# Kernel tuning notes

Measured on AMD Instinct MI355X. Metric: run time of the kernel, lower is better.

The kernel has to match this reference:

```python
import jax, jax.numpy as jnp
import numpy as np

ALPHA = 0.2      # LeakyReLU negative slope
NEG_INF = -9e15  # mask value from the original code

def setup_inputs() -> dict:
    key = jax.random.key(0)
    k1, k2, k3, k4 = jax.random.split(key, 4)
    B, M, F_IN, F_OUT = 16, 2048, 128, 64
    h = jax.random.normal(k1, (B, M, F_IN), dtype=jnp.float32)
    adj = jax.random.randint(k2, (B, M, M), 0, 2, dtype=jnp.int32)
    W = jax.random.normal(k3, (F_IN, F_OUT), dtype=jnp.float32) * 0.1
    a = jax.random.normal(k4, (2 * F_OUT, 1), dtype=jnp.float32) * 0.1
    return {"h": h, "adj": adj, "W": W, "a": a}

def reference(h, adj, W, a):
    # h: [B,M,Fin], adj: [B,M,M], W: [Fin,E], a: [2E,1]
    Wh = jnp.matmul(h, W)                      # [B,M,E]
    E = Wh.shape[-1]
    a1, a2 = a[:E, 0], a[E:, 0]
    # decompose a^T [Wh_i || Wh_j] = (Wh_i . a1) + (Wh_j . a2)
    f1 = Wh @ a1                               # [B,M] (source/query term)
    f2 = Wh @ a2                               # [B,M] (target/key term)
    e = jax.nn.leaky_relu(f1[:, :, None] + f2[:, None, :], negative_slope=ALPHA)  # [B,M,M]
    scores = jnp.where(adj > 0, e, NEG_INF)
    attn = jax.nn.softmax(scores, axis=-1)     # [B,M,M]  (dropout p=0 / eval mode)
    h_prime = jnp.matmul(attn, Wh)             # [B,M,E]
    return jax.nn.elu(h_prime)                 # concat=True branch
```

## Files before the change

kernel.cpp:

```cpp
#include <hip/hip_runtime.h>


#define M_     2048
#define FIN_   128
#define F_     64
#define ALPHA_ 0.2f
#define HS_    132
#define WT_    132

typedef float  float4_ __attribute__((ext_vector_type(4)));
typedef short  short8  __attribute__((ext_vector_type(8)));
typedef int    int4_   __attribute__((ext_vector_type(4)));
typedef unsigned int u32x4 __attribute__((ext_vector_type(4)));
typedef unsigned short u16;
typedef unsigned int   u32;

static __device__ __forceinline__ u32 cvtpk(float lo, float hi) {
    u32 r;
    asm("v_cvt_pk_bf16_f32 %0, %1, %2" : "=v"(r) : "v"(lo), "v"(hi));
    return r;
}

static __device__ __forceinline__ int4_ ntload4(const int* p) {
    return __builtin_nontemporal_load((const int4_*)p);
}

__global__ __launch_bounds__(256, 4) void k_prep(
    const float* __restrict__ h, const float* __restrict__ W,
    const float* __restrict__ a, u16* __restrict__ hbf,
    float* __restrict__ f1all, float* __restrict__ f2all)
{
    __shared__ float a_s[2 * F_];
    __shared__ float wa1[FIN_], wa2[FIN_];
    __shared__ float hs[32 * HS_];

    const int tid = threadIdx.x;
    const u32 bid = blockIdx.x;
    const u32 lg  = (bid & 7) * 128 + (bid >> 3);
    const int b   = lg >> 6;
    const int t   = lg & 63;

    if (tid < 128) a_s[tid] = a[tid];

    const int tok = tid >> 3, f0 = (tid & 7) * 16;
    const float* hp = h + ((size_t)(b * M_ + t * 32 + tok)) * FIN_ + f0;
    float4_ x0 = *(const float4_*)hp;
    float4_ x1 = *(const float4_*)(hp + 4);
    float4_ x2 = *(const float4_*)(hp + 8);
    float4_ x3 = *(const float4_*)(hp + 12);
    __syncthreads();

    if (tid < FIN_) {
        float s1 = 0.f, s2 = 0.f;
#pragma unroll 8
        for (int n = 0; n < F_; ++n) {
            float wv = W[tid * F_ + n];
            s1 += wv * a_s[n];
            s2 += wv * a_s[F_ + n];
        }
        wa1[tid] = s1;
        wa2[tid] = s2;
    }

    float* hr = hs + tok * HS_ + f0;
    *(float4_*)(hr)      = x0;
    *(float4_*)(hr + 4)  = x1;
    *(float4_*)(hr + 8)  = x2;
    *(float4_*)(hr + 12) = x3;
    __syncthreads();

    {
        const int l = tid & 63, lc = l & 15, q = l >> 4;
        const int nt0 = (tid >> 6) * 2;
        u32x4* ob = (u32x4*)hbf + ((size_t)(b * 64 + t)) * 8 * 64;
#pragma unroll
        for (int ni = 0; ni < 2; ++ni) {
            const int nt = nt0 + ni;
            const float* cp = hs + (q * 8) * HS_ + nt * 16 + lc;
            u32x4 wv;
            wv[0] = cvtpk(cp[0 * HS_], cp[1 * HS_]);
            wv[1] = cvtpk(cp[2 * HS_], cp[3 * HS_]);
            wv[2] = cvtpk(cp[4 * HS_], cp[5 * HS_]);
            wv[3] = cvtpk(cp[6 * HS_], cp[7 * HS_]);
            ob[nt * 64 + l] = wv;
        }
    }

    {
        const int r = tid >> 3, k0 = (tid & 7) * 16;
        const float* rp = hs + r * HS_ + k0;
        float s1 = 0.f, s2 = 0.f;
#pragma unroll
        for (int k = 0; k < 16; ++k) {
            s1 += rp[k] * wa1[k0 + k];
            s2 += rp[k] * wa2[k0 + k];
        }
        s1 += __shfl_xor(s1, 1, 64); s2 += __shfl_xor(s2, 1, 64);
        s1 += __shfl_xor(s1, 2, 64); s2 += __shfl_xor(s2, 2, 64);
        s1 += __shfl_xor(s1, 4, 64); s2 += __shfl_xor(s2, 4, 64);
        if ((tid & 7) == 0) {
            f1all[b * M_ + t * 32 + r] = s1;
            f2all[b * M_ + t * 32 + r] = s2;
        }
    }
}

__global__ __launch_bounds__(256, 2) void k_main(
    const int* __restrict__ adj, const u16* __restrict__ hbf,
    const float* __restrict__ f1all, const float* __restrict__ f2all,
    const float* __restrict__ W, float* __restrict__ out)
{
    __shared__ char  dyn[64 * WT_ * 4];
    __shared__ float dens[64];

    u32x4* lbuf = (u32x4*)dyn;
    float* f2s  = (float*)(dyn + 16384);
    float* Tsum = (float*)dyn;

    const int tid  = threadIdx.x;
    const int w    = tid >> 6;
    const int l    = tid & 63;
    const int lc   = l & 15;
    const int quad = l >> 4;

    const u32 bid = blockIdx.x;
    const u32 lg  = (bid & 7) * 64 + (bid >> 3);
    const int b   = lg >> 5;
    const int i0  = (lg & 31) * 64;

    {
        const int o = tid * 8;
        float4_ v0 = *(const float4_*)(f2all + b * M_ + o);
        float4_ v1 = *(const float4_*)(f2all + b * M_ + o + 4);
        *(float4_*)(f2s + o)     = v0;
        *(float4_*)(f2s + o + 4) = v1;
    }

    const float f1r = f1all[b * M_ + i0 + w * 16 + lc];
    const int* aprow = adj + ((size_t)(b * M_ + i0 + w * 16 + lc)) * M_ + quad * 8;
    const u32x4* hbs = (const u32x4*)hbf + (size_t)b * 32768;

    {
        u32x4 s0 = hbs[tid];
        u32x4 s1 = hbs[256 + tid];
        lbuf[tid]       = s0;
        lbuf[256 + tid] = s1;
    }
    int4_ aA0 = ntload4(aprow);
    int4_ aA1 = ntload4(aprow + 4);
    int4_ aB0 = ntload4(aprow + 32);
    int4_ aB1 = ntload4(aprow + 36);

    __syncthreads();

    float denacc = 0.f;
    float4_ acc[8];
#pragma unroll
    for (int nt = 0; nt < 8; ++nt) acc[nt] = (float4_){0.f, 0.f, 0.f, 0.f};

#define SC(GE, GO, AE, AO, IDX)                                 \
        {                                                       \
            float xe = f1r + (GE); xe = fmaxf(xe, ALPHA_ * xe); \
            float xo = f1r + (GO); xo = fmaxf(xo, ALPHA_ * xo); \
            float ee = ((AE) > 0) ? __expf(xe) : 0.f;           \
            float eo = ((AO) > 0) ? __expf(xo) : 0.f;           \
            u32 pk = cvtpk(ee, eo);                             \
            d += __uint_as_float(pk << 16);                     \
            d += __uint_as_float(pk & 0xFFFF0000u);             \
            pw[IDX] = pk;                                       \
        }

#define STAGE(T, A0, A1)                                                      \
    {                                                                         \
        const int ts = ((T) < 63) ? (T) + 1 : 63;                             \
        const int tp = ((T) < 62) ? (T) + 2 : 63;                             \
        u32x4 s0 = hbs[ts * 512 + tid];                                       \
        u32x4 s1 = hbs[ts * 512 + 256 + tid];                                 \
        __builtin_amdgcn_sched_barrier(0);                                    \
        const u32x4* lc_ = lbuf + ((T) & 1) * 512;                            \
        u32x4 bb[8];                                                          \
        _Pragma("unroll")                                                     \
        for (int nt = 0; nt < 8; ++nt) bb[nt] = lc_[nt * 64 + l];             \
        float4_ g0 = *(const float4_*)(f2s + (T) * 32 + quad * 8);            \
        float4_ g1 = *(const float4_*)(f2s + (T) * 32 + quad * 8 + 4);        \
        u32x4 pw;                                                             \
        float d = 0.f;                                                        \
        SC(g0[0], g0[1], A0[0], A0[1], 0)                                     \
        SC(g0[2], g0[3], A0[2], A0[3], 1)                                     \
        SC(g1[0], g1[1], A1[0], A1[1], 2)                                     \
        SC(g1[2], g1[3], A1[2], A1[3], 3)                                     \
        denacc += d;                                                          \
        const short8 af = __builtin_bit_cast(short8, pw);                     \
        A0 = ntload4(aprow + tp * 32);                                        \
        A1 = ntload4(aprow + tp * 32 + 4);                                    \
        _Pragma("unroll")                                                     \
        for (int nt = 0; nt < 8; ++nt)                                        \
            acc[nt] = __builtin_amdgcn_mfma_f32_16x16x32_bf16(                \
                af, __builtin_bit_cast(short8, bb[nt]), acc[nt], 0, 0, 0);    \
        __builtin_amdgcn_sched_barrier(0);                                    \
        u32x4* ln_ = lbuf + (((T) + 1) & 1) * 512;                            \
        ln_[tid]       = s0;                                                  \
        ln_[256 + tid] = s1;                                                  \
        asm volatile("s_waitcnt lgkmcnt(0)" ::: "memory");                    \
        __builtin_amdgcn_s_barrier();                                         \
        __builtin_amdgcn_sched_barrier(0);                                    \
    }

    for (int o2 = 0; o2 < 32; ++o2) {
        STAGE(2 * o2,     aA0, aA1)
        STAGE(2 * o2 + 1, aB0, aB1)
    }
#undef STAGE
#undef SC

    denacc += __shfl_xor(denacc, 16, 64);
    denacc += __shfl_xor(denacc, 32, 64);
    if (quad == 0) dens[w * 16 + lc] = denacc;
    __syncthreads();

#pragma unroll
    for (int nt = 0; nt < 8; ++nt)
#pragma unroll
        for (int mm = 0; mm < 4; ++mm)
            Tsum[(w * 16 + quad * 4 + mm) * WT_ + nt * 16 + lc] = acc[nt][mm];
    __syncthreads();

#pragma unroll
    for (int rr = 0; rr < 2; ++rr) {
        const int r  = (tid >> 3) + rr * 32;
        const int n0 = (tid & 7) * 8;
        const float den  = dens[r];
        const float rden = (den > 0.f) ? (1.f / den) : 0.f;
        float u[8];
#pragma unroll
        for (int nn = 0; nn < 8; ++nn) u[nn] = 0.f;
#pragma unroll 4
        for (int k = 0; k < FIN_; ++k) {
            const float tv = Tsum[r * WT_ + k];
            float4_ wv0 = *(const float4_*)(W + k * F_ + n0);
            float4_ wv1 = *(const float4_*)(W + k * F_ + n0 + 4);
            u[0] += tv * wv0[0]; u[1] += tv * wv0[1];
            u[2] += tv * wv0[2]; u[3] += tv * wv0[3];
            u[4] += tv * wv1[0]; u[5] += tv * wv1[1];
            u[6] += tv * wv1[2]; u[7] += tv * wv1[3];
        }
        float4_ o0, o1;
#pragma unroll
        for (int nn = 0; nn < 8; ++nn) {
            float hp = u[nn] * rden;
            float o  = hp > 0.f ? hp : expm1f(hp);
            if (nn < 4) o0[nn] = o; else o1[nn - 4] = o;
        }
        float* op = out + ((size_t)(b * M_ + i0 + r)) * F_ + n0;
        *(float4_*)op       = o0;
        *(float4_*)(op + 4) = o1;
    }
}

extern "C" void kernel_launch(void* const* d_in, const int* in_sizes, int n_in,
                              void* d_out, int out_size, void* d_ws, size_t ws_size,
                              hipStream_t stream)
{
    (void)out_size; (void)ws_size;
    const float* h  = (const float*)d_in[0];
    const int* adjp = (const int*)d_in[1];
    const float* Wp = (const float*)d_in[2];
    const float* ap = (const float*)d_in[3];
    for (int i = 0; i < n_in; ++i) {
        long s = in_sizes[i];
        if      (s == 4194304L)  h    = (const float*)d_in[i];
        else if (s == 67108864L) adjp = (const int*)d_in[i];
        else if (s == 8192L)     Wp   = (const float*)d_in[i];
        else if (s == 128L)      ap   = (const float*)d_in[i];
    }
    u16*   hbf   = (u16*)d_ws;
    float* f1all = (float*)((char*)d_ws + (8u << 20));
    float* f2all = f1all + 16 * M_;
    k_prep<<<1024, 256, 0, stream>>>(h, Wp, ap, hbf, f1all, f2all);
    k_main<<<512, 256, 0, stream>>>(adjp, hbf, f1all, f2all, Wp, (float*)d_out);
}
```

Measured before the change: 416.7 us.

## Pack adjacency into bitmask in separate kernel and stage mask in LDS

A new k_pack kernel reads the int32 adjacency matrix once and compresses each run of 32 entries into a u32 bitmask. The main kernel then loads its 64-row mask tile into LDS up front and tests bits, instead of streaming int32 adjacency rows inside the pipelined loop. This takes the large global adjacency reads out of the compute loop, but adds a kernel launch and a full pass over adj, so the total adj traffic stays about the same and the pass is now serialized before k_main.

```diff
diff --git a/kernel.cpp b/kernel.cpp
--- a/kernel.cpp
+++ b/kernel.cpp
@@ -7,6 +7,7 @@
 #define ALPHA_ 0.2f
 #define HS_    132
 #define WT_    132
+#define MS_    68
 
 typedef float  float4_ __attribute__((ext_vector_type(4)));
 typedef short  short8  __attribute__((ext_vector_type(8)));
@@ -105,16 +106,37 @@
     }
 }
 
+__global__ __launch_bounds__(256, 4) void k_pack(
+    const int* __restrict__ adj, u32* __restrict__ mask)
+{
+    u32 wi = blockIdx.x * 256 + threadIdx.x;
+#pragma unroll
+    for (int it = 0; it < 4; ++it, wi += 2048 * 256) {
+        const int* ap = adj + (size_t)wi * 32;
+        u32 m = 0;
+#pragma unroll
+        for (int c = 0; c < 8; ++c) {
+            int4_ v = ntload4(ap + c * 4);
+            m |= (v[0] > 0 ? 1u : 0u) << (c * 4 + 0);
+            m |= (v[1] > 0 ? 1u : 0u) << (c * 4 + 1);
+            m |= (v[2] > 0 ? 1u : 0u) << (c * 4 + 2);
+            m |= (v[3] > 0 ? 1u : 0u) << (c * 4 + 3);
+        }
+        mask[wi] = m;
+    }
+}
+
 __global__ __launch_bounds__(256, 2) void k_main(
-    const int* __restrict__ adj, const u16* __restrict__ hbf,
+    const u32* __restrict__ mask, const u16* __restrict__ hbf,
     const float* __restrict__ f1all, const float* __restrict__ f2all,
     const float* __restrict__ W, float* __restrict__ out)
 {
-    __shared__ char  dyn[64 * WT_ * 4];
+    __shared__ char  dyn[41984];
     __shared__ float dens[64];
 
     u32x4* lbuf = (u32x4*)dyn;
     float* f2s  = (float*)(dyn + 16384);
+    u32*   mlds = (u32*)(dyn + 24576);
     float* Tsum = (float*)dyn;
 
     const int tid  = threadIdx.x;
@@ -135,10 +157,20 @@
         *(float4_*)(f2s + o)     = v0;
         *(float4_*)(f2s + o + 4) = v1;
     }
+    {
+        const u32* mrow = mask + ((size_t)(b * M_ + i0)) * 64;
+#pragma unroll
+        for (int c = 0; c < 4; ++c) {
+            const int gw = c * 1024 + tid * 4;
+            u32x4 v = *(const u32x4*)(mrow + gw);
+            *(u32x4*)(mlds + (gw >> 6) * MS_ + (gw & 63)) = v;
+        }
+    }
 
     const float f1r = f1all[b * M_ + i0 + w * 16 + lc];
-    const int* aprow = adj + ((size_t)(b * M_ + i0 + w * 16 + lc)) * M_ + quad * 8;
     const u32x4* hbs = (const u32x4*)hbf + (size_t)b * 32768;
+    const u32* mrd = mlds + (w * 16 + lc) * MS_;
+    const int  msh = quad * 8;
 
     {
         u32x4 s0 = hbs[tid];
@@ -146,10 +178,6 @@
         lbuf[tid]       = s0;
         lbuf[256 + tid] = s1;
     }
-    int4_ aA0 = ntload4(aprow);
-    int4_ aA1 = ntload4(aprow + 4);
-    int4_ aB0 = ntload4(aprow + 32);
-    int4_ aB1 = ntload4(aprow + 36);
 
     __syncthreads();
 
@@ -158,22 +186,21 @@
 #pragma unroll
     for (int nt = 0; nt < 8; ++nt) acc[nt] = (float4_){0.f, 0.f, 0.f, 0.f};
 
-#define SC(GE, GO, AE, AO, IDX)                                 \
+#define SC(GE, GO, BE, BO, IDX)                                 \
         {                                                       \
             float xe = f1r + (GE); xe = fmaxf(xe, ALPHA_ * xe); \
             float xo = f1r + (GO); xo = fmaxf(xo, ALPHA_ * xo); \
-            float ee = ((AE) > 0) ? __expf(xe) : 0.f;           \
-            float eo = ((AO) > 0) ? __expf(xo) : 0.f;           \
+            float ee = (mq & (1u << (BE))) ? __expf(xe) : 0.f;  \
+            float eo = (mq & (1u << (BO))) ? __expf(xo) : 0.f;  \
             u32 pk = cvtpk(ee, eo);                             \
             d += __uint_as_float(pk << 16);                     \
             d += __uint_as_float(pk & 0xFFFF0000u);             \
             pw[IDX] = pk;                                       \
         }
 
-#define STAGE(T, A0, A1)                                                      \
+#define STAGE(T)                                                              \
     {                                                                         \
         const int ts = ((T) < 63) ? (T) + 1 : 63;                             \
-        const int tp = ((T) < 62) ? (T) + 2 : 63;                             \
         u32x4 s0 = hbs[ts * 512 + tid];                                       \
         u32x4 s1 = hbs[ts * 512 + 256 + tid];                                 \
         __builtin_amdgcn_sched_barrier(0);                                    \
@@ -181,18 +208,17 @@
         u32x4 bb[8];                                                          \
         _Pragma("unroll")                                                     \
         for (int nt = 0; nt < 8; ++nt) bb[nt] = lc_[nt * 64 + l];             \
+        const u32 mq = mrd[T] >> msh;                                         \
         float4_ g0 = *(const float4_*)(f2s + (T) * 32 + quad * 8);            \
         float4_ g1 = *(const float4_*)(f2s + (T) * 32 + quad * 8 + 4);        \
         u32x4 pw;                                                             \
         float d = 0.f;                                                        \
-        SC(g0[0], g0[1], A0[0], A0[1], 0)                                     \
-        SC(g0[2], g0[3], A0[2], A0[3], 1)                                     \
-        SC(g1[0], g1[1], A1[0], A1[1], 2)                                     \
-        SC(g1[2], g1[3], A1[2], A1[3], 3)                                     \
+        SC(g0[0], g0[1], 0, 1, 0)                                             \
+        SC(g0[2], g0[3], 2, 3, 1)                                             \
+        SC(g1[0], g1[1], 4, 5, 2)                                             \
+        SC(g1[2], g1[3], 6, 7, 3)                                             \
         denacc += d;                                                          \
         const short8 af = __builtin_bit_cast(short8, pw);                     \
-        A0 = ntload4(aprow + tp * 32);                                        \
-        A1 = ntload4(aprow + tp * 32 + 4);                                    \
         _Pragma("unroll")                                                     \
         for (int nt = 0; nt < 8; ++nt)                                        \
             acc[nt] = __builtin_amdgcn_mfma_f32_16x16x32_bf16(                \
@@ -207,8 +233,8 @@
     }
 
     for (int o2 = 0; o2 < 32; ++o2) {
-        STAGE(2 * o2,     aA0, aA1)
-        STAGE(2 * o2 + 1, aB0, aB1)
+        STAGE(2 * o2)
+        STAGE(2 * o2 + 1)
     }
 #undef STAGE
 #undef SC
@@ -276,6 +302,8 @@
     u16*   hbf   = (u16*)d_ws;
     float* f1all = (float*)((char*)d_ws + (8u << 20));
     float* f2all = f1all + 16 * M_;
+    u32*   maskp = (u32*)((char*)d_ws + (16u << 20));
     k_prep<<<1024, 256, 0, stream>>>(h, Wp, ap, hbf, f1all, f2all);
-    k_main<<<512, 256, 0, stream>>>(adjp, hbf, f1all, f2all, Wp, (float*)d_out);
-}
+    k_pack<<<2048, 256, 0, stream>>>(adjp, maskp);
+    k_main<<<512, 256, 0, stream>>>(maskp, hbf, f1all, f2all, Wp, (float*)d_out);
+}
```

Result: slower. 523.3 us (+25.6%).
